# Kernel optimization log

Hardware: AMD Instinct MI355X
Metric: run time of the kernel (lower is better)

The kernel has to match this reference:

```python
import jax, jax.numpy as jnp
import numpy as np

B, S, HID = 1, 2048, 2048
H, KV, D = 32, 8, 64          # query heads, kv heads, head_dim
N_REP = H // KV
BASE = 10000.0


def rotate_half(x):
    x1, x2 = x[..., : D // 2], x[..., D // 2 :]
    return jnp.concatenate((-x2, x1), axis=-1)


def setup_inputs() -> dict:
    key = jax.random.key(0)
    ks = jax.random.split(key, 6)
    std = 0.02
    return {
        "hidden_states": jax.random.normal(ks[0], (B, S, HID), jnp.float32),
        "position_ids": jnp.broadcast_to(jnp.arange(S, dtype=jnp.int32), (B, S)),
        "powers": jax.random.normal(ks[1], (D // 2,), jnp.float32),
        "Wq": jax.random.normal(ks[2], (H * D, HID), jnp.float32) * std,
        "Wk": jax.random.normal(ks[3], (KV * D, HID), jnp.float32) * std,
        "Wv": jax.random.normal(ks[4], (KV * D, HID), jnp.float32) * std,
        "Wo": jax.random.normal(ks[5], (HID, H * D), jnp.float32) * std,
    }


def reference(hidden_states, position_ids, powers, Wq, Wk, Wv, Wo):
    bsz, q_len, _ = hidden_states.shape

    # QKV projections (no bias)
    q = (hidden_states @ Wq.T).reshape(bsz, q_len, H, D).transpose(0, 2, 1, 3)   # [B,H,S,D]
    k = (hidden_states @ Wk.T).reshape(bsz, q_len, KV, D).transpose(0, 2, 1, 3)  # [B,KV,S,D]
    v = (hidden_states @ Wv.T).reshape(bsz, q_len, KV, D).transpose(0, 2, 1, 3)

    # Learnable RoPE: inv_freq = base ** (-sigmoid(powers))
    inv_freq = 1.0 / (BASE ** jax.nn.sigmoid(powers))                 # [D/2]
    freqs = position_ids.astype(jnp.float32)[:, :, None] * inv_freq  # [B,S,D/2]
    emb = jnp.concatenate((freqs, freqs), axis=-1)                   # [B,S,D]
    cos = jnp.cos(emb)[:, None, :, :]                                # [B,1,S,D]
    sin = jnp.sin(emb)[:, None, :, :]

    q = q * cos + rotate_half(q) * sin
    k = k * cos + rotate_half(k) * sin

    # GQA: repeat_interleave kv heads
    k = jnp.repeat(k, N_REP, axis=1)  # [B,H,S,D]
    v = jnp.repeat(v, N_REP, axis=1)

    scores = jnp.einsum("bhqd,bhkd->bhqk", q, k) / np.sqrt(D).astype(np.float32)
    # additive causal mask (module is_causal=True)
    pos = jnp.arange(q_len)
    causal = jnp.where(pos[:, None] >= pos[None, :], 0.0, jnp.finfo(jnp.float32).min)
    scores = scores + causal

    probs = jax.nn.softmax(scores.astype(jnp.float32), axis=-1).astype(q.dtype)
    attn = jnp.einsum("bhqk,bhkd->bhqd", probs, v)                   # [B,H,S,D]
    attn = attn.transpose(0, 2, 1, 3).reshape(bsz, q_len, H * D)
    return attn @ Wo.T
```

## Files before the change

kernel.cpp:

```cpp
#include <hip/hip_runtime.h>

typedef unsigned short u16;
typedef __attribute__((ext_vector_type(8))) short short8;
typedef __attribute__((ext_vector_type(4))) short s16x4;
typedef __attribute__((ext_vector_type(4))) float f32x4;
typedef __attribute__((ext_vector_type(16))) float f32x16;
typedef __attribute__((ext_vector_type(4))) unsigned u32x4;

#define S_LEN 2048
#define HID 2048
#define NQH 32
#define NKV 8
#define HD 64
#define QKVN 3072
#define SCLOG2 0.1803368801111204f

__device__ __forceinline__ short f2b(float f){
  unsigned u = __builtin_bit_cast(unsigned, f);
  u += 0x7fffu + ((u >> 16) & 1u);
  return (short)(u >> 16);
}
__device__ __forceinline__ float b2f(u16 v){
  unsigned u = ((unsigned)v) << 16;
  return __builtin_bit_cast(float, u);
}
__device__ __forceinline__ void gll16(const void* g, void* l){
  __builtin_amdgcn_global_load_lds((const __attribute__((address_space(1))) void*)g,
                                   (__attribute__((address_space(3))) void*)l, 16, 0, 0);
}
__device__ __forceinline__ unsigned cvtpk(float a, float b){
  unsigned r;
  asm("v_cvt_pk_bf16_f32 %0, %1, %2" : "=v"(r) : "v"(a), "v"(b));
  return r;
}
__device__ __forceinline__ void pswap(unsigned &a, unsigned &b){
  asm volatile("v_permlane32_swap_b32 %0, %1" : "+v"(a), "+v"(b));
}
__device__ __forceinline__ float ex2(float x){
  float r; asm("v_exp_f32 %0, %1" : "=v"(r) : "v"(x)); return r;
}

__global__ __launch_bounds__(256) void cvt_all(const float* __restrict__ s0,
                                               const float* __restrict__ s1,
                                               const float* __restrict__ s2,
                                               const float* __restrict__ s3,
                                               const float* __restrict__ s4,
                                               u16* __restrict__ d0, u16* __restrict__ d1,
                                               u16* __restrict__ d2, u16* __restrict__ d3,
                                               u16* __restrict__ d4,
                                               const int* __restrict__ pos,
                                               const float* __restrict__ powers,
                                               float* __restrict__ cost,
                                               float* __restrict__ sint){
  int i = blockIdx.x * 256 + threadIdx.x;
  if (i >= 1835008) {
    int j = i - 1835008;
    int s = j >> 5, d = j & 31;
    float p = (float)pos[s];
    float w = powers[d];
    float sig = 1.0f / (1.0f + expf(-w));
    float inv = powf(10000.0f, -sig);
    float f = p * inv;
    cost[j] = cosf(f);
    sint[j] = sinf(f);
    return;
  }
  const float* s; u16* d; int off;
  if      (i <  524288){ s = s0; d = d0; off = i; }
  else if (i < 1048576){ s = s1; d = d1; off = i -  524288; }
  else if (i < 1179648){ s = s2; d = d2; off = i - 1048576; }
  else if (i < 1310720){ s = s3; d = d3; off = i - 1179648; }
  else                 { s = s4; d = d4; off = i - 1310720; }
  const float4* s4p = (const float4*)s;
  float4 a = s4p[off*2], b = s4p[off*2+1];
  short8 o = { f2b(a.x), f2b(a.y), f2b(a.z), f2b(a.w),
               f2b(b.x), f2b(b.y), f2b(b.z), f2b(b.w) };
  *(short8*)(d + (size_t)off*8) = o;
}

template<int MODE>
__global__ __launch_bounds__(256) void gemm_bt(const u16* __restrict__ A,
                                               const u16* __restrict__ B0,
                                               const u16* __restrict__ B1,
                                               const u16* __restrict__ B2,
                                               int n1, int n2,
                                               void* __restrict__ Cout,
                                               u16* __restrict__ vtOut,
                                               int M, int Ntot, int K,
                                               const float* __restrict__ cost,
                                               const float* __restrict__ sint){
  __shared__ alignas(16) u16 sA[2][128*64];
  __shared__ alignas(16) u16 sB[2][128*64];
  const int tid = threadIdx.x, lane = tid & 63, wv = tid >> 6;
  const int wr = wv >> 1, wc = wv & 1;
  const int m0 = blockIdx.y * 128, n0 = blockIdx.x * 128;
  const int lr = lane & 15, lg = lane >> 4;

  const u16* B;
  if (n0 < n1)      B = B0 + (size_t)n0 * K;
  else if (n0 < n2) B = B1 + (size_t)(n0 - n1) * K;
  else              B = B2 + (size_t)(n0 - n2) * K;

  const int sRow = tid >> 3;
  const int sCol = ((tid & 7) ^ (sRow & 7)) * 8;
  const u16* Arow = A + (size_t)(m0 + sRow)*K + sCol;
  const u16* Brow = B + (size_t)sRow*K + sCol;

  f32x4 acc[4][4] = {};
  const int NT = K >> 6;

  #pragma unroll
  for (int i = 0; i < 4; ++i) {
    gll16(Arow + (size_t)i*32*K, (char*)&sA[0][0] + i*4096 + tid*16);
    gll16(Brow + (size_t)i*32*K, (char*)&sB[0][0] + i*4096 + tid*16);
  }
  __syncthreads();

  for (int t = 0; t < NT; ++t) {
    const int cur = t & 1;
    if (t + 1 < NT) {
      const int kn = (t + 1) << 6;
      #pragma unroll
      for (int i = 0; i < 4; ++i) {
        gll16(Arow + (size_t)i*32*K + kn, (char*)&sA[cur^1][0] + i*4096 + tid*16);
        gll16(Brow + (size_t)i*32*K + kn, (char*)&sB[cur^1][0] + i*4096 + tid*16);
      }
    }
    const char* bA = (const char*)&sA[cur][0];
    const char* bB = (const char*)&sB[cur][0];
    #pragma unroll
    for (int kk = 0; kk < 64; kk += 32) {
      short8 af[4], bfr[4];
      #pragma unroll
      for (int m = 0; m < 4; ++m)
        af[m] = *(const short8*)(bA + (wr*64 + m*16 + lr)*128 + ((((kk>>3) + lg) ^ (lr & 7)) << 4));
      #pragma unroll
      for (int n = 0; n < 4; ++n)
        bfr[n] = *(const short8*)(bB + (wc*64 + n*16 + lr)*128 + ((((kk>>3) + lg) ^ (lr & 7)) << 4));
      #pragma unroll
      for (int m = 0; m < 4; ++m)
        #pragma unroll
        for (int n = 0; n < 4; ++n)
          acc[m][n] = __builtin_amdgcn_mfma_f32_16x16x32_bf16(af[m], bfr[n], acc[m][n], 0, 0, 0);
    }
    asm volatile("s_waitcnt vmcnt(0)" ::: "memory");
    __builtin_amdgcn_s_barrier();
  }

  if (MODE == 0 && n0 >= 2560) {
    #pragma unroll
    for (int n = 0; n < 4; ++n) {
      const int colv = n0 - 2560 + wc*64 + n*16 + lr;
      #pragma unroll
      for (int m = 0; m < 4; ++m) {
        const int row = m0 + wr*64 + m*16 + lg*4;
        s16x4 o = { f2b(acc[m][n][0]), f2b(acc[m][n][1]),
                    f2b(acc[m][n][2]), f2b(acc[m][n][3]) };
        *(s16x4*)&vtOut[(size_t)colv*S_LEN + row] = o;
      }
    }
  } else if (MODE == 0) {
    const float qsc = (n0 < n1) ? SCLOG2 : 1.0f;
    #pragma unroll
    for (int m = 0; m < 4; ++m)
      #pragma unroll
      for (int r = 0; r < 4; ++r) {
        int row = m0 + wr*64 + m*16 + lg*4 + r;
        float c0 = cost[row*32 + lr],      s0 = sint[row*32 + lr];
        float c1 = cost[row*32 + 16 + lr], s1 = sint[row*32 + 16 + lr];
        float x0 = acc[m][0][r], x1 = acc[m][1][r];
        float x2 = acc[m][2][r], x3 = acc[m][3][r];
        float o0 = (x0*c0 - x2*s0)*qsc, o2 = (x2*c0 + x0*s0)*qsc;
        float o1 = (x1*c1 - x3*s1)*qsc, o3 = (x3*c1 + x1*s1)*qsc;
        u16* cp = (u16*)Cout + (size_t)row*Ntot + n0 + wc*64 + lr;
        cp[0]  = (u16)f2b(o0);
        cp[16] = (u16)f2b(o1);
        cp[32] = (u16)f2b(o2);
        cp[48] = (u16)f2b(o3);
      }
  } else {
    #pragma unroll
    for (int m = 0; m < 4; ++m)
      #pragma unroll
      for (int n = 0; n < 4; ++n)
        #pragma unroll
        for (int r = 0; r < 4; ++r) {
          int row = m0 + wr*64 + m*16 + lg*4 + r;
          int col = n0 + wc*64 + n*16 + lr;
          ((float*)Cout)[(size_t)row*Ntot + col] = acc[m][n][r];
        }
  }
}

__global__ __launch_bounds__(256) void flash_attn(const u16* __restrict__ qkv,
                                                  const u16* __restrict__ vt,
                                                  u16* __restrict__ attn){
  __shared__ alignas(16) u16 sK[4][64*64];
  __shared__ alignas(16) u16 sVT[4][64*64];
  const int tid = threadIdx.x, lane = tid & 63, w = tid >> 6;
  const int bid = blockIdx.x + (blockIdx.y << 4);
  int chunk, h;
  if (bid < 256) { chunk = 15 - (bid & 15); h = bid >> 4; }
  else           { int b2 = bid - 256; chunk = b2 & 15; h = 16 + (b2 >> 4); }
  const int kvh = h >> 2;
  const int l5 = lane & 31, hi = lane >> 5;
  const int l8g = lane >> 3, b8 = lane & 7;
  const int colOff = (b8 ^ (l8g & 7)) * 8;
  const int q0w = chunk*128 + w*32;
  const int qg = q0w + l5;

  const u16* srcK = qkv + (size_t)(16*w + l8g)*QKVN + HID + kvh*HD + colOff;
  const u16* srcV = vt + (size_t)(kvh*HD + 16*w + l8g)*S_LEN + colOff;

  auto STAGE = [&](int t, int buf){
    const int kn = t*64;
    char* dK = (char*)&sK[buf][0]  + w*2048;
    char* dV = (char*)&sVT[buf][0] + w*2048;
    gll16(srcK + (size_t)kn*QKVN,       dK);
    gll16(srcK + (size_t)(kn+8)*QKVN,   dK + 1024);
    gll16(srcV + kn,                    dV);
    gll16(srcV + kn + (size_t)8*S_LEN,  dV + 1024);
  };

  short8 qf[4];
  #pragma unroll
  for (int cc = 0; cc < 4; ++cc)
    qf[cc] = *(const short8*)&qkv[(size_t)(q0w + l5)*QKVN + h*HD + cc*16 + hi*8];

  f32x16 accO[2] = {};
  float l_part = 0.f;
  const int nt = 2*chunk + 2;

  STAGE(0, 0);
  STAGE(1, 1);

  auto QK = [&](const char* bK, f32x16 (&st)[2]){
    __builtin_amdgcn_s_setprio(1);
    #pragma unroll
    for (int sub = 0; sub < 2; ++sub) {
      short8 kf[4];
      #pragma unroll
      for (int cc = 0; cc < 4; ++cc)
        kf[cc] = *(const short8*)(bK + (sub*32 + l5)*128 + (((cc*2 + hi) ^ (l5 & 7))*16));
      f32x16 za = {}, zb = {};
      za = __builtin_amdgcn_mfma_f32_32x32x16_bf16(kf[0], qf[0], za, 0, 0, 0);
      zb = __builtin_amdgcn_mfma_f32_32x32x16_bf16(kf[1], qf[1], zb, 0, 0, 0);
      za = __builtin_amdgcn_mfma_f32_32x32x16_bf16(kf[2], qf[2], za, 0, 0, 0);
      zb = __builtin_amdgcn_mfma_f32_32x32x16_bf16(kf[3], qf[3], zb, 0, 0, 0);
      st[sub] = za + zb;
    }
    __builtin_amdgcn_s_setprio(0);
  };

  auto SMPV = [&](int kt, const char* bV, f32x16 (&st)[2]){
    #pragma unroll
    for (int sub = 0; sub < 2; ++sub) {
      f32x16& z = st[sub];
      if (kt + 63 > q0w) {
        #pragma unroll
        for (int r = 0; r < 16; ++r) {
          const int k = kt + sub*32 + (r&3) + 8*(r>>2) + 4*hi;
          float e = ex2(z[r]);
          z[r] = (k > qg) ? 0.f : e;
        }
      } else {
        #pragma unroll
        for (int r = 0; r < 16; ++r) z[r] = ex2(z[r]);
      }
      float s0 = (z[0]+z[1]) + (z[2]+z[3]);
      float s1 = (z[4]+z[5]) + (z[6]+z[7]);
      float s2 = (z[8]+z[9]) + (z[10]+z[11]);
      float s3 = (z[12]+z[13]) + (z[14]+z[15]);
      l_part += (s0+s1) + (s2+s3);
    }
    short8 pa[4];
    #pragma unroll
    for (int sub = 0; sub < 2; ++sub) {
      unsigned a0 = cvtpk(st[sub][0],  st[sub][1]);
      unsigned c0 = cvtpk(st[sub][2],  st[sub][3]);
      unsigned b0 = cvtpk(st[sub][4],  st[sub][5]);
      unsigned d0 = cvtpk(st[sub][6],  st[sub][7]);
      pswap(a0, b0); pswap(c0, d0);
      u32x4 w0 = {a0, c0, b0, d0};
      pa[sub*2] = __builtin_bit_cast(short8, w0);
      unsigned a1 = cvtpk(st[sub][8],  st[sub][9]);
      unsigned c1 = cvtpk(st[sub][10], st[sub][11]);
      unsigned b1 = cvtpk(st[sub][12], st[sub][13]);
      unsigned d1 = cvtpk(st[sub][14], st[sub][15]);
      pswap(a1, b1); pswap(c1, d1);
      u32x4 w1 = {a1, c1, b1, d1};
      pa[sub*2+1] = __builtin_bit_cast(short8, w1);
    }
    __builtin_amdgcn_s_setprio(1);
    #pragma unroll
    for (int s4 = 0; s4 < 4; ++s4)
      #pragma unroll
      for (int db = 0; db < 2; ++db) {
        short8 vf = *(const short8*)(bV + (db*32 + l5)*128 + (((s4*2 + hi) ^ (l5 & 7))*16));
        accO[db] = __builtin_amdgcn_mfma_f32_32x32x16_bf16(vf, pa[s4], accO[db], 0, 0, 0);
      }
    __builtin_amdgcn_s_setprio(0);
  };

  for (int t = 0; t < nt; t += 2) {
    const int ktA = t*64, ktB = ktA + 64;
    asm volatile("s_waitcnt vmcnt(0)" ::: "memory");
    __builtin_amdgcn_s_barrier();
    if (t + 2 < nt) {
      STAGE(t + 2, (t + 2) & 3);
      STAGE(t + 3, (t + 3) & 3);
    }

    const bool doA = (ktA <= q0w + 31);
    const bool doB = (ktB <= q0w + 31);
    const char* bKA = (const char*)&sK[t & 3][0];
    const char* bVA = (const char*)&sVT[t & 3][0];
    const char* bKB = (const char*)&sK[(t + 1) & 3][0];
    const char* bVB = (const char*)&sVT[(t + 1) & 3][0];

    f32x16 stA[2], stB[2];
    if (doA) QK(bKA, stA);
    if (doB) QK(bKB, stB);
    if (doA) SMPV(ktA, bVA, stA);
    if (doB) SMPV(ktB, bVB, stB);
  }

  const float l_run = l_part + __shfl_xor(l_part, 32);
  const float invl = 1.0f / l_run;
  #pragma unroll
  for (int db = 0; db < 2; ++db)
    #pragma unroll
    for (int g2 = 0; g2 < 4; ++g2) {
      s16x4 o = { f2b(accO[db][g2*4+0]*invl), f2b(accO[db][g2*4+1]*invl),
                  f2b(accO[db][g2*4+2]*invl), f2b(accO[db][g2*4+3]*invl) };
      *(s16x4*)&attn[(size_t)(q0w + l5)*HID + h*HD + db*32 + g2*8 + hi*4] = o;
    }
}

extern "C" void kernel_launch(void* const* d_in, const int* in_sizes, int n_in,
                              void* d_out, int out_size, void* d_ws, size_t ws_size,
                              hipStream_t stream){
  const float* hs     = (const float*)d_in[0];
  const int*   pos    = (const int*)d_in[1];
  const float* powers = (const float*)d_in[2];
  const float* Wq     = (const float*)d_in[3];
  const float* Wk     = (const float*)d_in[4];
  const float* Wv     = (const float*)d_in[5];
  const float* Wo     = (const float*)d_in[6];
  float* out = (float*)d_out;

  char* ws = (char*)d_ws;
  auto take = [&](size_t bytes){ void* p = ws; ws += (bytes + 255) & ~(size_t)255; return p; };
  u16* hs_b  = (u16*)take((size_t)S_LEN*HID*2);
  u16* wq_b  = (u16*)take((size_t)HID*HID*2);
  u16* wk_b  = (u16*)take((size_t)NKV*HD*HID*2);
  u16* wv_b  = (u16*)take((size_t)NKV*HD*HID*2);
  u16* wo_b  = (u16*)take((size_t)HID*HID*2);
  u16* qkv   = (u16*)take((size_t)S_LEN*QKVN*2);
  u16* vt    = (u16*)take((size_t)NKV*HD*S_LEN*2);
  u16* attnb = (u16*)take((size_t)S_LEN*HID*2);
  float* cost = (float*)take((size_t)S_LEN*32*4);
  float* sint = (float*)take((size_t)S_LEN*32*4);

  cvt_all<<<7424, 256, 0, stream>>>(hs, Wq, Wk, Wv, Wo,
                                    hs_b, wq_b, wk_b, wv_b, wo_b,
                                    pos, powers, cost, sint);

  gemm_bt<0><<<dim3(QKVN/128, S_LEN/128), 256, 0, stream>>>(
      hs_b, wq_b, wk_b, wv_b, HID, HID + NKV*HD, qkv, vt,
      S_LEN, QKVN, HID, cost, sint);

  flash_attn<<<dim3(16, NQH), 256, 0, stream>>>(qkv, vt, attnb);

  gemm_bt<1><<<dim3(HID/128, S_LEN/128), 256, 0, stream>>>(
      attnb, wo_b, wo_b, wo_b, 1<<28, 1<<29, out, nullptr,
      S_LEN, HID, HID, nullptr, nullptr);
}
```

Baseline: 132.8 us.

## Split long causal attention chunks across two blocks with a combine pass

For the query chunks 8-15, which have the most causal KV tiles, the work is split into two KV halves, each handled by a separate block. Each half writes unnormalized fp32 partial outputs and row sums, and a new combine kernel adds them and normalizes. The grid goes from 512 to 768 blocks, with a table ordering the work longest first, to balance load across CUs. The cost is an extra kernel launch plus fp32 partial-output traffic. The merge uses no max rescaling, which relies on the existing kernel using a fixed scale without a running max.

```diff
diff --git a/kernel.cpp b/kernel.cpp
--- a/kernel.cpp
+++ b/kernel.cpp
@@ -194,15 +194,23 @@
 
 __global__ __launch_bounds__(256) void flash_attn(const u16* __restrict__ qkv,
                                                   const u16* __restrict__ vt,
-                                                  u16* __restrict__ attn){
+                                                  u16* __restrict__ attn,
+                                                  float* __restrict__ pO,
+                                                  float* __restrict__ pL){
   __shared__ alignas(16) u16 sK[4][64*64];
   __shared__ alignas(16) u16 sVT[4][64*64];
+  static const int c_tab[24] = {7,15,15,14,14,6,13,13,12,12,5,11,11,
+                                10,10,4,9,9,8,8,3,2,1,0};
+  static const int s_tab[24] = {2,0,1,0,1,2,0,1,0,1,2,0,1,
+                                0,1,2,0,1,0,1,2,2,2,2};
   const int tid = threadIdx.x, lane = tid & 63, w = tid >> 6;
-  const int bid = blockIdx.x + (blockIdx.y << 4);
-  int chunk, h;
-  if (bid < 256) { chunk = 15 - (bid & 15); h = bid >> 4; }
-  else           { int b2 = bid - 256; chunk = b2 & 15; h = 16 + (b2 >> 4); }
-  const int kvh = h >> 2;
+  const int h = blockIdx.x, kvh = h >> 2;
+  const int chunk = c_tab[blockIdx.y];
+  const int sl = s_tab[blockIdx.y];
+  int t0, ntb;
+  if (sl == 2) { t0 = 0; ntb = 2*chunk + 2; }
+  else         { t0 = sl*(chunk + 1); ntb = chunk + 1; }
+
   const int l5 = lane & 31, hi = lane >> 5;
   const int l8g = lane >> 3, b8 = lane & 7;
   const int colOff = (b8 ^ (l8g & 7)) * 8;
@@ -229,10 +237,9 @@
 
   f32x16 accO[2] = {};
   float l_part = 0.f;
-  const int nt = 2*chunk + 2;
-
-  STAGE(0, 0);
-  STAGE(1, 1);
+
+  STAGE(t0, 0);
+  STAGE(t0 + 1, 1);
 
   auto QK = [&](const char* bK, f32x16 (&st)[2]){
     __builtin_amdgcn_s_setprio(1);
@@ -302,21 +309,19 @@
     __builtin_amdgcn_s_setprio(0);
   };
 
-  for (int t = 0; t < nt; t += 2) {
-    const int ktA = t*64, ktB = ktA + 64;
+  for (int lt = 0; lt < ntb; lt += 2) {
     asm volatile("s_waitcnt vmcnt(0)" ::: "memory");
     __builtin_amdgcn_s_barrier();
-    if (t + 2 < nt) {
-      STAGE(t + 2, (t + 2) & 3);
-      STAGE(t + 3, (t + 3) & 3);
-    }
-
+    if (lt + 2 < ntb) STAGE(t0 + lt + 2, (lt + 2) & 3);
+    if (lt + 3 < ntb) STAGE(t0 + lt + 3, (lt + 3) & 3);
+
+    const int ktA = (t0 + lt)*64, ktB = ktA + 64;
     const bool doA = (ktA <= q0w + 31);
-    const bool doB = (ktB <= q0w + 31);
-    const char* bKA = (const char*)&sK[t & 3][0];
-    const char* bVA = (const char*)&sVT[t & 3][0];
-    const char* bKB = (const char*)&sK[(t + 1) & 3][0];
-    const char* bVB = (const char*)&sVT[(t + 1) & 3][0];
+    const bool doB = (lt + 1 < ntb) && (ktB <= q0w + 31);
+    const char* bKA = (const char*)&sK[lt & 3][0];
+    const char* bVA = (const char*)&sVT[lt & 3][0];
+    const char* bKB = (const char*)&sK[(lt + 1) & 3][0];
+    const char* bVB = (const char*)&sVT[(lt + 1) & 3][0];
 
     f32x16 stA[2], stB[2];
     if (doA) QK(bKA, stA);
@@ -326,15 +331,52 @@
   }
 
   const float l_run = l_part + __shfl_xor(l_part, 32);
-  const float invl = 1.0f / l_run;
+  if (sl == 2) {
+    const float invl = 1.0f / l_run;
+    #pragma unroll
+    for (int db = 0; db < 2; ++db)
+      #pragma unroll
+      for (int g2 = 0; g2 < 4; ++g2) {
+        s16x4 o = { f2b(accO[db][g2*4+0]*invl), f2b(accO[db][g2*4+1]*invl),
+                    f2b(accO[db][g2*4+2]*invl), f2b(accO[db][g2*4+3]*invl) };
+        *(s16x4*)&attn[(size_t)(q0w + l5)*HID + h*HD + db*32 + g2*8 + hi*4] = o;
+      }
+  } else {
+    const int slot = (h*8 + (chunk - 8))*2 + sl;
+    const int row = w*32 + l5;
+    float* po = pO + (size_t)slot*128*64 + (size_t)row*64;
+    #pragma unroll
+    for (int db = 0; db < 2; ++db)
+      #pragma unroll
+      for (int g2 = 0; g2 < 4; ++g2) {
+        f32x4 v = { accO[db][g2*4+0], accO[db][g2*4+1],
+                    accO[db][g2*4+2], accO[db][g2*4+3] };
+        *(f32x4*)&po[db*32 + g2*8 + hi*4] = v;
+      }
+    if (lane < 32)
+      pL[(size_t)slot*128 + row] = l_run;
+  }
+}
+
+__global__ __launch_bounds__(256) void combine(const float* __restrict__ pO,
+                                               const float* __restrict__ pL,
+                                               u16* __restrict__ attn){
+  int i = blockIdx.x * 256 + threadIdx.x;
+  int d8 = i & 7;
+  int row = (i >> 3) & 127;
+  int cc = (i >> 10) & 7;
+  int h = i >> 13;
+  int slot0 = (h*8 + cc)*2;
+  float l = pL[(size_t)slot0*128 + row] + pL[(size_t)(slot0+1)*128 + row];
+  const float* p0 = pO + (size_t)slot0*128*64 + (size_t)row*64 + d8*8;
+  const float* p1 = p0 + 128*64;
+  const float inv = 1.0f / l;
+  short8 o;
   #pragma unroll
-  for (int db = 0; db < 2; ++db)
-    #pragma unroll
-    for (int g2 = 0; g2 < 4; ++g2) {
-      s16x4 o = { f2b(accO[db][g2*4+0]*invl), f2b(accO[db][g2*4+1]*invl),
-                  f2b(accO[db][g2*4+2]*invl), f2b(accO[db][g2*4+3]*invl) };
-      *(s16x4*)&attn[(size_t)(q0w + l5)*HID + h*HD + db*32 + g2*8 + hi*4] = o;
-    }
+  for (int j = 0; j < 8; ++j)
+    o[j] = f2b((p0[j] + p1[j]) * inv);
+  const int q = (8 + cc)*128 + row;
+  *(short8*)&attn[(size_t)q*HID + h*HD + d8*8] = o;
 }
 
 extern "C" void kernel_launch(void* const* d_in, const int* in_sizes, int n_in,
@@ -361,6 +403,8 @@
   u16* attnb = (u16*)take((size_t)S_LEN*HID*2);
   float* cost = (float*)take((size_t)S_LEN*32*4);
   float* sint = (float*)take((size_t)S_LEN*32*4);
+  float* pO   = (float*)take((size_t)NQH*8*2*128*64*4);
+  float* pL   = (float*)take((size_t)NQH*8*2*128*4);
 
   cvt_all<<<7424, 256, 0, stream>>>(hs, Wq, Wk, Wv, Wo,
                                     hs_b, wq_b, wk_b, wv_b, wo_b,
@@ -370,7 +414,8 @@
       hs_b, wq_b, wk_b, wv_b, HID, HID + NKV*HD, qkv, vt,
       S_LEN, QKVN, HID, cost, sint);
 
-  flash_attn<<<dim3(16, NQH), 256, 0, stream>>>(qkv, vt, attnb);
+  flash_attn<<<dim3(NQH, 24), 256, 0, stream>>>(qkv, vt, attnb, pO, pL);
+  combine<<<1024, 256, 0, stream>>>(pO, pL, attnb);
 
   gemm_bt<1><<<dim3(HID/128, S_LEN/128), 256, 0, stream>>>(
       attnb, wo_b, wo_b, wo_b, 1<<28, 1<<29, out, nullptr,
```

Result: no change. 133.1 us (+0.2%).
